# Kernel tuning notes

Measured on AMD Instinct MI355X. Metric: run time of the kernel, lower is better.

## Reference

```python
import jax, jax.numpy as jnp
import numpy as np

B, N, D_IN, D_OUT = 2, 2048, 2048, 2048
H, G = 16, 4            # num_heads, n_kv_groups
HD = D_OUT // H         # head_dim = 128
REP = H // G            # query heads per kv head = 4


def setup_inputs() -> dict:
    key = jax.random.key(0)
    ks = jax.random.split(key, 6)
    s = lambda fan_in: 1.0 / np.sqrt(fan_in)
    return {
        "x": jax.random.normal(ks[0], (B, N, D_IN), jnp.float32),
        "Wq": jax.random.normal(ks[1], (D_IN, D_OUT), jnp.float32) * s(D_IN),
        "Wk": jax.random.normal(ks[2], (D_IN, G * HD), jnp.float32) * s(D_IN),
        "Wv": jax.random.normal(ks[3], (D_IN, G * HD), jnp.float32) * s(D_IN),
        "Wo": jax.random.normal(ks[4], (D_OUT, D_OUT), jnp.float32) * s(D_OUT),
        "bo": jnp.zeros((D_OUT,), jnp.float32),
    }


def reference(x, Wq, Wk, Wv, Wo, bo):
    b, n, _ = x.shape
    # projections
    q = (x @ Wq).reshape(b, n, G, REP, HD)   # query heads grouped: h = g*REP + r
    k = (x @ Wk).reshape(b, n, G, HD)
    v = (x @ Wv).reshape(b, n, G, HD)
    # grouped attention scores; KV broadcast over REP instead of repeat_kv
    scores = jnp.einsum('bqgrd,bkgd->bgrqk', q, k)  # [b,G,REP,N,N]
    causal = jnp.tril(jnp.ones((n, n), bool))       # allowed positions
    scores = jnp.where(causal, scores, -jnp.inf)
    w = jax.nn.softmax(scores / np.float32(np.sqrt(HD)), axis=-1)
    ctx = jnp.einsum('bgrqk,bkgd->bqgrd', w, v).reshape(b, n, D_OUT)
    return ctx @ Wo + bo
```

## Files before the change

kernel.cpp:

```cpp
#include <hip/hip_runtime.h>
#include <stdint.h>

typedef __attribute__((ext_vector_type(8))) __bf16 bf16x8;
typedef __attribute__((ext_vector_type(4))) float f32x4;
typedef __attribute__((ext_vector_type(4))) short short4v;

static constexpr int SEQ  = 2048;
static constexpr int DQKV = 3072;
static constexpr int HD   = 128;

__device__ __forceinline__ short f2bf(float f) {
  unsigned u = __builtin_bit_cast(unsigned, f);
  u += 0x7fffu + ((u >> 16) & 1u);
  return (short)(u >> 16);
}

__device__ __forceinline__ unsigned pack2(float a, float b) {
  return (unsigned)(unsigned short)f2bf(a) | ((unsigned)(unsigned short)f2bf(b) << 16);
}

__device__ __forceinline__ void gl_lds16(const void* g, void* l) {
  __builtin_amdgcn_global_load_lds(
      (const __attribute__((address_space(1))) void*)g,
      (__attribute__((address_space(3))) void*)l, 16, 0, 0);
}

__global__ __launch_bounds__(256)
void prep_kernel(const float* __restrict__ x, const float* __restrict__ Wq,
                 const float* __restrict__ Wk, const float* __restrict__ Wv,
                 const float* __restrict__ Wo,
                 short* __restrict__ xb, short* __restrict__ WqkvT,
                 short* __restrict__ WoT) {
  int blk = blockIdx.x, tid = threadIdx.x;
  if (blk < 8192) {
    int i = blk * 256 + tid;
    float4 v = reinterpret_cast<const float4*>(x)[i];
    short4v o;
    o[0] = f2bf(v.x); o[1] = f2bf(v.y); o[2] = f2bf(v.z); o[3] = f2bf(v.w);
    *reinterpret_cast<short4v*>(xb + (size_t)i * 4) = o;
    return;
  }
  blk -= 8192;
  __shared__ float tile[32][33];
  const float* in; short* out; int C, bx, by;
  if (blk < 4096)      { in = Wq; out = WqkvT;                     C = 2048; bx = blk & 63; by = blk >> 6; }
  else if (blk < 5120) { int t = blk - 4096; in = Wk; out = WqkvT + (size_t)2048 * 2048; C = 512; bx = t & 15; by = t >> 4; }
  else if (blk < 6144) { int t = blk - 5120; in = Wv; out = WqkvT + (size_t)2560 * 2048; C = 512; bx = t & 15; by = t >> 4; }
  else                 { int t = blk - 6144; in = Wo; out = WoT;   C = 2048; bx = t & 63; by = t >> 6; }
  const int R = 2048;
  int c0 = bx * 32, r0 = by * 32, tx = tid & 31, ty = tid >> 5;
  for (int i = 0; i < 4; i++)
    tile[ty + i * 8][tx] = in[(size_t)(r0 + ty + i * 8) * C + c0 + tx];
  __syncthreads();
  for (int i = 0; i < 4; i++)
    out[(size_t)(c0 + ty + i * 8) * R + r0 + tx] = f2bf(tile[tx][ty + i * 8]);
}

__global__ __launch_bounds__(256) void transpose_v_kernel(const short* __restrict__ qkv,
                                                          short* __restrict__ vT) {
  __shared__ short tile[32][33];
  int n0 = blockIdx.x * 32, c0 = blockIdx.y * 32, b = blockIdx.z;
  int tx = threadIdx.x & 31, ty = threadIdx.x >> 5;
  for (int i = 0; i < 4; i++)
    tile[ty + i * 8][tx] = qkv[(size_t)(b * SEQ + n0 + ty + i * 8) * DQKV + 2560 + c0 + tx];
  __syncthreads();
  for (int i = 0; i < 4; i++)
    vT[(size_t)(b * 512 + c0 + ty + i * 8) * SEQ + n0 + tx] = tile[tx][ty + i * 8];
}

template <int F32OUT>
__global__ __launch_bounds__(256)
void gemm_bt_kernel(const short* __restrict__ A, const short* __restrict__ BT,
                    void* __restrict__ Cout, const float* __restrict__ bias,
                    int M, int N, int K, int qcols, float qscale) {
  __shared__ __align__(16) short As[8192];
  __shared__ __align__(16) short Bs[8192];
  const int tid = threadIdx.x, lane = tid & 63, w = tid >> 6;
  const int l15 = lane & 15, quad = lane >> 4, q8 = quad * 8;
  const int row0 = blockIdx.y * 128, col0 = blockIdx.x * 128;
  const int wm = (w >> 1) * 64, wn = (w & 1) * 64;
  f32x4 acc[4][4] = {};
  const short* ga0 = A  + (size_t)(row0 + w * 16 + (lane >> 2)) * K + (lane & 3) * 8;
  const short* gb0 = BT + (size_t)(col0 + w * 16 + (lane >> 2)) * K + (lane & 3) * 8;
  for (int kt = 0; kt < K; kt += 64) {
    for (int s = 0; s < 2; s++) {
      gl_lds16(ga0 + kt + s * 32,                  As + s * 4096 + w * 512);
      gl_lds16(ga0 + (size_t)64 * K + kt + s * 32, As + s * 4096 + 2048 + w * 512);
      gl_lds16(gb0 + kt + s * 32,                  Bs + s * 4096 + w * 512);
      gl_lds16(gb0 + (size_t)64 * K + kt + s * 32, Bs + s * 4096 + 2048 + w * 512);
    }
    __syncthreads();
    for (int s = 0; s < 2; s++) {
      bf16x8 af[4], bfr[4];
      for (int i = 0; i < 4; i++)
        af[i] = *reinterpret_cast<const bf16x8*>(As + s * 4096 + (wm + i * 16 + l15) * 32 + q8);
      for (int j = 0; j < 4; j++)
        bfr[j] = *reinterpret_cast<const bf16x8*>(Bs + s * 4096 + (wn + j * 16 + l15) * 32 + q8);
      for (int i = 0; i < 4; i++)
        for (int j = 0; j < 4; j++)
          acc[i][j] = __builtin_amdgcn_mfma_f32_16x16x32_bf16(af[i], bfr[j], acc[i][j], 0, 0, 0);
    }
    __syncthreads();
  }
  if (F32OUT) {
    float* C = (float*)Cout;
    for (int j = 0; j < 4; j++) {
      int col = col0 + wn + j * 16 + l15;
      float bv = bias[col];
      for (int i = 0; i < 4; i++)
        for (int r = 0; r < 4; r++)
          C[(size_t)(row0 + wm + i * 16 + quad * 4 + r) * N + col] = acc[i][j][r] + bv;
    }
  } else {
    short* C = (short*)Cout;
    for (int j = 0; j < 4; j++) {
      int col = col0 + wn + j * 16 + l15;
      float sc = (col < qcols) ? qscale : 1.0f;
      for (int i = 0; i < 4; i++)
        for (int r = 0; r < 4; r++)
          C[(size_t)(row0 + wm + i * 16 + quad * 4 + r) * N + col] = f2bf(acc[i][j][r] * sc);
    }
  }
}

__global__ __launch_bounds__(256, 2)
void attn_kernel(const short* __restrict__ qkv, const short* __restrict__ vT,
                 short* __restrict__ ctx) {
  __shared__ __align__(16) short Ks[16384];
  __shared__ __align__(16) short Vs[16384];
  __shared__ __align__(16) short Ps[4096];
  const int tid = threadIdx.x, lane = tid & 63, w = tid >> 6;
  const int l15 = lane & 15, quad = lane >> 4, q8 = quad * 8;
  const int idx = blockIdx.x;
  const int p = idx >> 5, h = (idx >> 1) & 15, b = idx & 1, g = h >> 2;
  const int qtA = 31 - p, qtB = p;

  bf16x8 qf[2][4];
  for (int seg = 0; seg < 2; seg++) {
    const int qt = seg ? qtB : qtA;
    const short* gq = qkv + (size_t)(b * SEQ + qt * 64 + w * 16 + l15) * DQKV + h * HD + q8;
    for (int ds = 0; ds < 4; ds++)
      qf[seg][ds] = *reinterpret_cast<const bf16x8*>(gq + ds * 32);
  }
  bf16x8 ones;
  for (int i = 0; i < 8; i++) ones[i] = __builtin_bit_cast(__bf16, (short)0x3F80);

  f32x4 acco[8] = {};
  f32x4 accl = {};

  auto stage = [&](int buf, int kt) {
    const short* gk = qkv + (size_t)(b * SEQ + kt * 64 + w * 16 + (lane >> 2)) * DQKV +
                      2048 + g * HD + (lane & 3) * 8;
    for (int ks = 0; ks < 4; ks++)
      gl_lds16(gk + ks * 32, Ks + buf * 8192 + ks * 2048 + w * 512);
    for (int c = 0; c < 2; c++)
      for (int ih = 0; ih < 2; ih++)
        gl_lds16(vT + (size_t)(b * 512 + g * HD + ih * 64 + w * 16 + (lane >> 2)) * SEQ +
                     kt * 64 + c * 32 + (lane & 3) * 8,
                 Vs + buf * 8192 + c * 4096 + ih * 2048 + w * 512);
  };

  const int lenA = qtA + 1;
  const int total = lenA + qtB + 1;
  stage(0, 0);
  for (int t = 0; t < total; t++) {
    const int seg = (t >= lenA);
    const int kt = seg ? (t - lenA) : t;
    const int qt = seg ? qtB : qtA;
    const int cur = t & 1;
    __syncthreads();
    if (t + 1 < total) {
      const int nkt = (t + 1 >= lenA) ? (t + 1 - lenA) : (t + 1);
      stage(cur ^ 1, nkt);
    }

    const short* Kb = Ks + cur * 8192;
    const short* Vb = Vs + cur * 8192;

    f32x4 accs[4] = {};
    for (int ds = 0; ds < 4; ds++)
      for (int j = 0; j < 4; j++) {
        bf16x8 kf = *reinterpret_cast<const bf16x8*>(Kb + ds * 2048 + (j * 16 + l15) * 32 + q8);
        accs[j] = __builtin_amdgcn_mfma_f32_16x16x32_bf16(kf, qf[seg][ds], accs[j], 0, 0, 0);
      }

    if (kt == qt) {
      const int q = w * 16 + l15;
      for (int j = 0; j < 4; j++)
        for (int r = 0; r < 4; r++)
          if (j * 16 + quad * 4 + r > q) accs[j][r] = -1e38f;
    }

    for (int j = 0; j < 4; j++) {
      float p0 = exp2f(accs[j][0]), p1 = exp2f(accs[j][1]);
      float p2 = exp2f(accs[j][2]), p3 = exp2f(accs[j][3]);
      unsigned u0 = __builtin_bit_cast(unsigned, p0), u1 = __builtin_bit_cast(unsigned, p1);
      unsigned u2 = __builtin_bit_cast(unsigned, p2), u3 = __builtin_bit_cast(unsigned, p3);
      uint2 dd = make_uint2((u0 >> 16) | (u1 & 0xffff0000u),
                            (u2 >> 16) | (u3 & 0xffff0000u));
      const int chw = (2 * j + (quad >> 1)) ^ (l15 & 7);
      *reinterpret_cast<uint2*>(Ps + w * 1024 + l15 * 64 + chw * 8 + (quad & 1) * 4) = dd;
    }
    asm volatile("s_waitcnt lgkmcnt(0)" ::: "memory");

    for (int c = 0; c < 2; c++) {
      const int chr = (4 * c + quad) ^ (l15 & 7);
      bf16x8 pf = *reinterpret_cast<const bf16x8*>(Ps + w * 1024 + l15 * 64 + chr * 8);
      accl = __builtin_amdgcn_mfma_f32_16x16x32_bf16(ones, pf, accl, 0, 0, 0);
      for (int nt = 0; nt < 8; nt++) {
        bf16x8 vf = *reinterpret_cast<const bf16x8*>(Vb + c * 4096 + (nt * 16 + l15) * 32 + q8);
        acco[nt] = __builtin_amdgcn_mfma_f32_16x16x32_bf16(vf, pf, acco[nt], 0, 0, 0);
      }
    }

    if (kt == qt) {
      const float invl = 1.f / accl[0];
      const size_t row = (size_t)(b * SEQ + qt * 64 + w * 16 + l15);
      for (int nt = 0; nt < 8; nt++) {
        uint2 dd = make_uint2(pack2(acco[nt][0] * invl, acco[nt][1] * invl),
                              pack2(acco[nt][2] * invl, acco[nt][3] * invl));
        *reinterpret_cast<uint2*>(ctx + row * 2048 + h * HD + nt * 16 + quad * 4) = dd;
      }
      for (int nt = 0; nt < 8; nt++) acco[nt] = f32x4{0.f, 0.f, 0.f, 0.f};
      accl = f32x4{0.f, 0.f, 0.f, 0.f};
    }
  }
}

extern "C" void kernel_launch(void* const* d_in, const int* in_sizes, int n_in,
                              void* d_out, int out_size, void* d_ws, size_t ws_size,
                              hipStream_t stream) {
  const float* x  = (const float*)d_in[0];
  const float* Wq = (const float*)d_in[1];
  const float* Wk = (const float*)d_in[2];
  const float* Wv = (const float*)d_in[3];
  const float* Wo = (const float*)d_in[4];
  const float* bo = (const float*)d_in[5];
  float* out = (float*)d_out;

  const float sc2 = 0.08838834764831845f * 1.4426950408889634f;

  short* xb    = (short*)d_ws;
  short* WqkvT = xb    + (size_t)4096 * 2048;
  short* WoT   = WqkvT + (size_t)3072 * 2048;
  short* qkv   = WoT   + (size_t)2048 * 2048;
  short* vT    = qkv   + (size_t)4096 * 3072;
  short* ctx   = vT    + (size_t)1024 * 2048;

  prep_kernel<<<dim3(18432), dim3(256), 0, stream>>>(x, Wq, Wk, Wv, Wo, xb, WqkvT, WoT);
  gemm_bt_kernel<0><<<dim3(24, 32), dim3(256), 0, stream>>>(xb, WqkvT, qkv, nullptr,
                                                            4096, 3072, 2048, 2048, sc2);
  transpose_v_kernel<<<dim3(64, 16, 2), dim3(256), 0, stream>>>(qkv, vT);
  attn_kernel<<<dim3(512), dim3(256), 0, stream>>>(qkv, vT, ctx);
  gemm_bt_kernel<1><<<dim3(16, 32), dim3(256), 0, stream>>>(ctx, WoT, out, bo,
                                                            4096, 2048, 2048, 0, 1.0f);
}
```

Before: 299.4 us.

## Restructure attention to 32x32 MFMA with split-K waves and register P

Rewrites the attention kernel to use 32x32x16 MFMA tiles. Each wave now handles a 32-query by 32-key quadrant, and two key-half waves are reduced through LDS at the end of each query tile. V is loaded straight from global into registers instead of being staged in LDS. P is converted to a B operand with permlane32_swap rather than a round trip through LDS, and the row sum is accumulated with scalar adds instead of a ones-MFMA. The aim is to cut LDS traffic and instruction count, at the cost of uncached global V loads on the critical path, an extra barrier and reduction per query tile, and more register pressure.

```diff
diff --git a/kernel.cpp b/kernel.cpp
--- a/kernel.cpp
+++ b/kernel.cpp
@@ -3,7 +3,9 @@
 
 typedef __attribute__((ext_vector_type(8))) __bf16 bf16x8;
 typedef __attribute__((ext_vector_type(4))) float f32x4;
+typedef __attribute__((ext_vector_type(16))) float f32x16;
 typedef __attribute__((ext_vector_type(4))) short short4v;
+typedef __attribute__((ext_vector_type(4))) unsigned uint4v;
 
 static constexpr int SEQ  = 2048;
 static constexpr int DQKV = 3072;
@@ -126,43 +128,32 @@
 __global__ __launch_bounds__(256, 2)
 void attn_kernel(const short* __restrict__ qkv, const short* __restrict__ vT,
                  short* __restrict__ ctx) {
-  __shared__ __align__(16) short Ks[16384];
-  __shared__ __align__(16) short Vs[16384];
-  __shared__ __align__(16) short Ps[4096];
+  __shared__ __align__(16) short Ks[2 * 8192];
+  __shared__ __align__(16) float Oex[2 * 4096];
+  __shared__ float lbuf[4 * 32];
   const int tid = threadIdx.x, lane = tid & 63, w = tid >> 6;
-  const int l15 = lane & 15, quad = lane >> 4, q8 = quad * 8;
+  const int l31 = lane & 31, hi = lane >> 5;
+  const int qh = w & 1, kh = w >> 1;
   const int idx = blockIdx.x;
   const int p = idx >> 5, h = (idx >> 1) & 15, b = idx & 1, g = h >> 2;
   const int qtA = 31 - p, qtB = p;
-
-  bf16x8 qf[2][4];
-  for (int seg = 0; seg < 2; seg++) {
-    const int qt = seg ? qtB : qtA;
-    const short* gq = qkv + (size_t)(b * SEQ + qt * 64 + w * 16 + l15) * DQKV + h * HD + q8;
-    for (int ds = 0; ds < 4; ds++)
-      qf[seg][ds] = *reinterpret_cast<const bf16x8*>(gq + ds * 32);
-  }
-  bf16x8 ones;
-  for (int i = 0; i < 8; i++) ones[i] = __builtin_bit_cast(__bf16, (short)0x3F80);
-
-  f32x4 acco[8] = {};
-  f32x4 accl = {};
-
-  auto stage = [&](int buf, int kt) {
-    const short* gk = qkv + (size_t)(b * SEQ + kt * 64 + w * 16 + (lane >> 2)) * DQKV +
-                      2048 + g * HD + (lane & 3) * 8;
-    for (int ks = 0; ks < 4; ks++)
-      gl_lds16(gk + ks * 32, Ks + buf * 8192 + ks * 2048 + w * 512);
-    for (int c = 0; c < 2; c++)
-      for (int ih = 0; ih < 2; ih++)
-        gl_lds16(vT + (size_t)(b * 512 + g * HD + ih * 64 + w * 16 + (lane >> 2)) * SEQ +
-                     kt * 64 + c * 32 + (lane & 3) * 8,
-                 Vs + buf * 8192 + c * 4096 + ih * 2048 + w * 512);
+  const int lenA = qtA + 1, total = lenA + qtB + 1;
+
+  auto stageK = [&](int buf, int kt) {
+    const short* gk = qkv + (size_t)(b * SEQ + kt * 64) * DQKV + 2048 + g * HD;
+#pragma unroll
+    for (int s = 0; s < 4; s++) {
+      const int r = w * 16 + s * 4 + (lane >> 4);
+      gl_lds16(gk + (size_t)r * DQKV + ((lane & 15) ^ (r & 7)) * 8,
+               Ks + buf * 8192 + (w * 16 + s * 4) * 128);
+    }
   };
 
-  const int lenA = qtA + 1;
-  const int total = lenA + qtB + 1;
-  stage(0, 0);
+  bf16x8 qf[8];
+  f32x16 o_acc[4] = {};
+  float lsum = 0.f;
+
+  stageK(0, 0);
   for (int t = 0; t < total; t++) {
     const int seg = (t >= lenA);
     const int kt = seg ? (t - lenA) : t;
@@ -171,58 +162,110 @@
     __syncthreads();
     if (t + 1 < total) {
       const int nkt = (t + 1 >= lenA) ? (t + 1 - lenA) : (t + 1);
-      stage(cur ^ 1, nkt);
-    }
+      stageK(cur ^ 1, nkt);
+    }
+    if (t == 0 || t == lenA) {
+      const short* gq = qkv + (size_t)(b * SEQ + qt * 64 + qh * 32 + l31) * DQKV + h * HD + hi * 8;
+#pragma unroll
+      for (int d = 0; d < 8; d++) qf[d] = *reinterpret_cast<const bf16x8*>(gq + d * 16);
+    }
+
+    bf16x8 vf[4][2];
+#pragma unroll
+    for (int dt = 0; dt < 4; dt++)
+#pragma unroll
+      for (int sub = 0; sub < 2; sub++)
+        vf[dt][sub] = *reinterpret_cast<const bf16x8*>(
+            vT + (size_t)(b * 512 + g * HD + dt * 32 + l31) * SEQ +
+            kt * 64 + (kh * 2 + sub) * 16 + hi * 8);
 
     const short* Kb = Ks + cur * 8192;
-    const short* Vb = Vs + cur * 8192;
-
-    f32x4 accs[4] = {};
-    for (int ds = 0; ds < 4; ds++)
-      for (int j = 0; j < 4; j++) {
-        bf16x8 kf = *reinterpret_cast<const bf16x8*>(Kb + ds * 2048 + (j * 16 + l15) * 32 + q8);
-        accs[j] = __builtin_amdgcn_mfma_f32_16x16x32_bf16(kf, qf[seg][ds], accs[j], 0, 0, 0);
+    f32x16 sa = {};
+#pragma unroll
+    for (int d = 0; d < 8; d++) {
+      bf16x8 kf = *reinterpret_cast<const bf16x8*>(
+          Kb + (kh * 32 + l31) * 128 + (((d * 2 + hi) ^ (l31 & 7)) * 8));
+      sa = __builtin_amdgcn_mfma_f32_32x32x16_bf16(kf, qf[d], sa, 0, 0, 0);
+    }
+
+    if (kt == qt) {
+      const int q = qh * 32 + l31;
+#pragma unroll
+      for (int r = 0; r < 16; r++)
+        if (kh * 32 + (r & 3) + 8 * (r >> 2) + 4 * hi > q) sa[r] = -1e38f;
+    }
+
+    float ps[16];
+#pragma unroll
+    for (int r = 0; r < 16; r++) ps[r] = exp2f(sa[r]);
+#pragma unroll
+    for (int r = 0; r < 16; r++) lsum += ps[r];
+    unsigned ub[4][2];
+#pragma unroll
+    for (int j = 0; j < 4; j++) {
+      unsigned a0 = __builtin_bit_cast(unsigned, ps[4 * j + 0]);
+      unsigned a1 = __builtin_bit_cast(unsigned, ps[4 * j + 1]);
+      unsigned a2 = __builtin_bit_cast(unsigned, ps[4 * j + 2]);
+      unsigned a3 = __builtin_bit_cast(unsigned, ps[4 * j + 3]);
+      ub[j][0] = (a0 >> 16) | (a1 & 0xffff0000u);
+      ub[j][1] = (a2 >> 16) | (a3 & 0xffff0000u);
+    }
+    bf16x8 pfrag[2];
+#pragma unroll
+    for (int sub = 0; sub < 2; sub++) {
+      auto s0 = __builtin_amdgcn_permlane32_swap((int)ub[2 * sub][0], (int)ub[2 * sub + 1][0], false, false);
+      auto s1 = __builtin_amdgcn_permlane32_swap((int)ub[2 * sub][1], (int)ub[2 * sub + 1][1], false, false);
+      uint4v uu;
+      uu[0] = (unsigned)s0[0]; uu[1] = (unsigned)s1[0];
+      uu[2] = (unsigned)s0[1]; uu[3] = (unsigned)s1[1];
+      pfrag[sub] = __builtin_bit_cast(bf16x8, uu);
+    }
+
+    __builtin_amdgcn_s_setprio(1);
+#pragma unroll
+    for (int dt = 0; dt < 4; dt++)
+#pragma unroll
+      for (int sub = 0; sub < 2; sub++)
+        o_acc[dt] = __builtin_amdgcn_mfma_f32_32x32x16_bf16(vf[dt][sub], pfrag[sub], o_acc[dt], 0, 0, 0);
+    __builtin_amdgcn_s_setprio(0);
+
+    if (kt == qt) {
+      float lp = lsum + __shfl_xor(lsum, 32, 64);
+      if (lane < 32) lbuf[w * 32 + l31] = lp;
+      if (w >= 2) {
+        float* oex = Oex + (w - 2) * 4096;
+#pragma unroll
+        for (int dt = 0; dt < 4; dt++)
+#pragma unroll
+          for (int rq = 0; rq < 4; rq++) {
+            f32x4 vv = {o_acc[dt][4 * rq + 0], o_acc[dt][4 * rq + 1],
+                        o_acc[dt][4 * rq + 2], o_acc[dt][4 * rq + 3]};
+            *reinterpret_cast<f32x4*>(oex + ((dt * 4 + rq) * 64 + lane) * 4) = vv;
+          }
       }
-
-    if (kt == qt) {
-      const int q = w * 16 + l15;
-      for (int j = 0; j < 4; j++)
-        for (int r = 0; r < 4; r++)
-          if (j * 16 + quad * 4 + r > q) accs[j][r] = -1e38f;
-    }
-
-    for (int j = 0; j < 4; j++) {
-      float p0 = exp2f(accs[j][0]), p1 = exp2f(accs[j][1]);
-      float p2 = exp2f(accs[j][2]), p3 = exp2f(accs[j][3]);
-      unsigned u0 = __builtin_bit_cast(unsigned, p0), u1 = __builtin_bit_cast(unsigned, p1);
-      unsigned u2 = __builtin_bit_cast(unsigned, p2), u3 = __builtin_bit_cast(unsigned, p3);
-      uint2 dd = make_uint2((u0 >> 16) | (u1 & 0xffff0000u),
-                            (u2 >> 16) | (u3 & 0xffff0000u));
-      const int chw = (2 * j + (quad >> 1)) ^ (l15 & 7);
-      *reinterpret_cast<uint2*>(Ps + w * 1024 + l15 * 64 + chw * 8 + (quad & 1) * 4) = dd;
-    }
-    asm volatile("s_waitcnt lgkmcnt(0)" ::: "memory");
-
-    for (int c = 0; c < 2; c++) {
-      const int chr = (4 * c + quad) ^ (l15 & 7);
-      bf16x8 pf = *reinterpret_cast<const bf16x8*>(Ps + w * 1024 + l15 * 64 + chr * 8);
-      accl = __builtin_amdgcn_mfma_f32_16x16x32_bf16(ones, pf, accl, 0, 0, 0);
-      for (int nt = 0; nt < 8; nt++) {
-        bf16x8 vf = *reinterpret_cast<const bf16x8*>(Vb + c * 4096 + (nt * 16 + l15) * 32 + q8);
-        acco[nt] = __builtin_amdgcn_mfma_f32_16x16x32_bf16(vf, pf, acco[nt], 0, 0, 0);
+      __syncthreads();
+      if (w < 2) {
+        const float invl = 1.f / (lp + lbuf[(w ^ 2) * 32 + l31]);
+        const float* oex = Oex + w * 4096;
+        const size_t row = (size_t)(b * SEQ + qt * 64 + qh * 32 + l31);
+#pragma unroll
+        for (int dt = 0; dt < 4; dt++)
+#pragma unroll
+          for (int rq = 0; rq < 4; rq++) {
+            f32x4 vv = *reinterpret_cast<const f32x4*>(oex + ((dt * 4 + rq) * 64 + lane) * 4);
+            float e0 = (o_acc[dt][4 * rq + 0] + vv[0]) * invl;
+            float e1 = (o_acc[dt][4 * rq + 1] + vv[1]) * invl;
+            float e2 = (o_acc[dt][4 * rq + 2] + vv[2]) * invl;
+            float e3 = (o_acc[dt][4 * rq + 3] + vv[3]) * invl;
+            uint2 dd = make_uint2(pack2(e0, e1), pack2(e2, e3));
+            *reinterpret_cast<uint2*>(ctx + row * 2048 + h * HD + dt * 32 + rq * 8 + hi * 4) = dd;
+          }
       }
-    }
-
-    if (kt == qt) {
-      const float invl = 1.f / accl[0];
-      const size_t row = (size_t)(b * SEQ + qt * 64 + w * 16 + l15);
-      for (int nt = 0; nt < 8; nt++) {
-        uint2 dd = make_uint2(pack2(acco[nt][0] * invl, acco[nt][1] * invl),
-                              pack2(acco[nt][2] * invl, acco[nt][3] * invl));
-        *reinterpret_cast<uint2*>(ctx + row * 2048 + h * HD + nt * 16 + quad * 4) = dd;
-      }
-      for (int nt = 0; nt < 8; nt++) acco[nt] = f32x4{0.f, 0.f, 0.f, 0.f};
-      accl = f32x4{0.f, 0.f, 0.f, 0.f};
+#pragma unroll
+      for (int dt = 0; dt < 4; dt++)
+#pragma unroll
+        for (int e = 0; e < 16; e++) o_acc[dt][e] = 0.f;
+      lsum = 0.f;
     }
   }
 }
```

New measurement: 310.3 us. +3.6%, slower.

## Rework attention kernel with 32x32 MFMA, split-K waves and software-pipelined QK/PV

Applied to the files above, without the earlier changes.

Rewrites the attention inner loop to use 32x32x16 MFMA tiles. The four waves are split into 2 query halves by 2 key halves. The P matrix is transposed in registers with permlane32_swap instead of a round-trip through LDS, and the row sum is kept as a scalar accumulator rather than computed with a ones-MFMA. QK^T for the next tile is software-pipelined against softmax/PV of the previous tile, with swizzled LDS layouts and setprio hints. The key-split partial outputs are reduced through shared memory at diagonal tiles. This adds extra barriers and LDS traffic at each diagonal, plus higher register pressure.

```diff
diff --git a/kernel.cpp b/kernel.cpp
--- a/kernel.cpp
+++ b/kernel.cpp
@@ -3,7 +3,9 @@
 
 typedef __attribute__((ext_vector_type(8))) __bf16 bf16x8;
 typedef __attribute__((ext_vector_type(4))) float f32x4;
+typedef __attribute__((ext_vector_type(16))) float f32x16;
 typedef __attribute__((ext_vector_type(4))) short short4v;
+typedef __attribute__((ext_vector_type(4))) unsigned uint4v;
 
 static constexpr int SEQ  = 2048;
 static constexpr int DQKV = 3072;
@@ -126,105 +128,187 @@
 __global__ __launch_bounds__(256, 2)
 void attn_kernel(const short* __restrict__ qkv, const short* __restrict__ vT,
                  short* __restrict__ ctx) {
-  __shared__ __align__(16) short Ks[16384];
-  __shared__ __align__(16) short Vs[16384];
-  __shared__ __align__(16) short Ps[4096];
+  __shared__ __align__(16) short Ks[2 * 8192];
+  __shared__ __align__(16) short Vs[2 * 8192];
+  __shared__ __align__(16) float Oex[2048];
+  __shared__ float lbuf[4 * 32];
   const int tid = threadIdx.x, lane = tid & 63, w = tid >> 6;
-  const int l15 = lane & 15, quad = lane >> 4, q8 = quad * 8;
+  const int l31 = lane & 31, hi = lane >> 5;
+  const int qh = w & 1, kh = w >> 1;
   const int idx = blockIdx.x;
   const int p = idx >> 5, h = (idx >> 1) & 15, b = idx & 1, g = h >> 2;
   const int qtA = 31 - p, qtB = p;
-
-  bf16x8 qf[2][4];
-  for (int seg = 0; seg < 2; seg++) {
-    const int qt = seg ? qtB : qtA;
-    const short* gq = qkv + (size_t)(b * SEQ + qt * 64 + w * 16 + l15) * DQKV + h * HD + q8;
-    for (int ds = 0; ds < 4; ds++)
-      qf[seg][ds] = *reinterpret_cast<const bf16x8*>(gq + ds * 32);
-  }
-  bf16x8 ones;
-  for (int i = 0; i < 8; i++) ones[i] = __builtin_bit_cast(__bf16, (short)0x3F80);
-
-  f32x4 acco[8] = {};
-  f32x4 accl = {};
+  const int lenA = qtA + 1;
 
   auto stage = [&](int buf, int kt) {
-    const short* gk = qkv + (size_t)(b * SEQ + kt * 64 + w * 16 + (lane >> 2)) * DQKV +
-                      2048 + g * HD + (lane & 3) * 8;
-    for (int ks = 0; ks < 4; ks++)
-      gl_lds16(gk + ks * 32, Ks + buf * 8192 + ks * 2048 + w * 512);
-    for (int c = 0; c < 2; c++)
-      for (int ih = 0; ih < 2; ih++)
-        gl_lds16(vT + (size_t)(b * 512 + g * HD + ih * 64 + w * 16 + (lane >> 2)) * SEQ +
-                     kt * 64 + c * 32 + (lane & 3) * 8,
-                 Vs + buf * 8192 + c * 4096 + ih * 2048 + w * 512);
+    const short* gk = qkv + (size_t)(b * SEQ + kt * 64) * DQKV + 2048 + g * HD;
+#pragma unroll
+    for (int s = 0; s < 4; s++) {
+      const int r = w * 16 + s * 4 + (lane >> 4);
+      gl_lds16(gk + (size_t)r * DQKV + ((lane & 15) ^ (r & 7)) * 8,
+               Ks + buf * 8192 + (w * 16 + s * 4) * 128);
+    }
+    const short* gv = vT + (size_t)(b * 512 + g * HD) * SEQ + kt * 64;
+#pragma unroll
+    for (int s = 0; s < 4; s++) {
+      const int r = w * 32 + s * 8 + (lane >> 3);
+      gl_lds16(gv + (size_t)r * SEQ + ((lane & 7) ^ (r & 7)) * 8,
+               Vs + buf * 8192 + (w * 32 + s * 8) * 64);
+    }
   };
 
-  const int lenA = qtA + 1;
-  const int total = lenA + qtB + 1;
+  bf16x8 qf[8];
+  f32x16 o_acc[4] = {};
+  float lsum = 0.f;
+  f32x16 saA, saB;
+  bf16x8 vfA[4][2], vfB[4][2];
+
+  auto loadQ = [&](int qt) {
+    const short* gq = qkv + (size_t)(b * SEQ + qt * 64 + qh * 32 + l31) * DQKV + h * HD + hi * 8;
+#pragma unroll
+    for (int d = 0; d < 8; d++) qf[d] = *reinterpret_cast<const bf16x8*>(gq + d * 16);
+  };
+
+#define PH1_BODY(T, CUR, SA, VF)                                                   \
+  {                                                                                \
+    if ((T) == 0 || (T) == lenA) loadQ(((T) >= lenA) ? qtB : qtA);                 \
+    const short* Kb_ = Ks + (CUR) * 8192;                                          \
+    const short* Vb_ = Vs + (CUR) * 8192;                                          \
+    f32x16 s0_ = {}, s1_ = {};                                                     \
+    __builtin_amdgcn_s_setprio(1);                                                 \
+    _Pragma("unroll")                                                              \
+    for (int d_ = 0; d_ < 4; d_++) {                                               \
+      bf16x8 kf0_ = *reinterpret_cast<const bf16x8*>(                              \
+          Kb_ + (kh * 32 + l31) * 128 + (((2 * d_ + hi) ^ (l31 & 7)) * 8));        \
+      bf16x8 kf1_ = *reinterpret_cast<const bf16x8*>(                              \
+          Kb_ + (kh * 32 + l31) * 128 + (((2 * (d_ + 4) + hi) ^ (l31 & 7)) * 8));  \
+      s0_ = __builtin_amdgcn_mfma_f32_32x32x16_bf16(kf0_, qf[d_], s0_, 0, 0, 0);   \
+      s1_ = __builtin_amdgcn_mfma_f32_32x32x16_bf16(kf1_, qf[d_ + 4], s1_, 0, 0, 0);\
+    }                                                                              \
+    __builtin_amdgcn_s_setprio(0);                                                 \
+    SA = s0_ + s1_;                                                                \
+    _Pragma("unroll")                                                              \
+    for (int dt_ = 0; dt_ < 4; dt_++)                                              \
+      _Pragma("unroll")                                                            \
+      for (int sub_ = 0; sub_ < 2; sub_++) {                                       \
+        const int kc_ = kh * 4 + sub_ * 2 + hi;                                    \
+        VF[dt_][sub_] = *reinterpret_cast<const bf16x8*>(                          \
+            Vb_ + (dt_ * 32 + l31) * 64 + ((kc_ ^ (l31 & 7)) * 8));                \
+      }                                                                            \
+  }
+
+#define PH2_BODY(T, SA, VF)                                                        \
+  {                                                                                \
+    const int seg_ = ((T) >= lenA);                                                \
+    const int ktc_ = seg_ ? (T) - lenA : (T);                                      \
+    const int qtc_ = seg_ ? qtB : qtA;                                             \
+    const bool diag_ = (ktc_ == qtc_);                                             \
+    if (diag_) {                                                                   \
+      const int q_ = qh * 32 + l31;                                                \
+      _Pragma("unroll")                                                            \
+      for (int r_ = 0; r_ < 16; r_++)                                              \
+        if (kh * 32 + (r_ & 3) + 8 * (r_ >> 2) + 4 * hi > q_) SA[r_] = -1e38f;     \
+    }                                                                              \
+    float ps_[16];                                                                 \
+    _Pragma("unroll")                                                              \
+    for (int r_ = 0; r_ < 16; r_++)                                                \
+      asm("v_exp_f32 %0, %1" : "=v"(ps_[r_]) : "v"(SA[r_]));                       \
+    _Pragma("unroll")                                                              \
+    for (int r_ = 0; r_ < 16; r_++) lsum += ps_[r_];                               \
+    unsigned ub_[4][2];                                                            \
+    _Pragma("unroll")                                                              \
+    for (int j_ = 0; j_ < 4; j_++) {                                               \
+      unsigned a0_ = __builtin_bit_cast(unsigned, ps_[4 * j_ + 0]);                \
+      unsigned a1_ = __builtin_bit_cast(unsigned, ps_[4 * j_ + 1]);                \
+      unsigned a2_ = __builtin_bit_cast(unsigned, ps_[4 * j_ + 2]);                \
+      unsigned a3_ = __builtin_bit_cast(unsigned, ps_[4 * j_ + 3]);                \
+      ub_[j_][0] = (a0_ >> 16) | (a1_ & 0xffff0000u);                              \
+      ub_[j_][1] = (a2_ >> 16) | (a3_ & 0xffff0000u);                              \
+    }                                                                              \
+    bf16x8 pf_[2];                                                                 \
+    _Pragma("unroll")                                                              \
+    for (int sub_ = 0; sub_ < 2; sub_++) {                                         \
+      auto s0_ = __builtin_amdgcn_permlane32_swap((int)ub_[2 * sub_][0],           \
+                                                  (int)ub_[2 * sub_ + 1][0], false, false); \
+      auto s1_ = __builtin_amdgcn_permlane32_swap((int)ub_[2 * sub_][1],           \
+                                                  (int)ub_[2 * sub_ + 1][1], false, false); \
+      uint4v uu_;                                                                  \
+      uu_[0] = (unsigned)s0_[0]; uu_[1] = (unsigned)s1_[0];                        \
+      uu_[2] = (unsigned)s0_[1]; uu_[3] = (unsigned)s1_[1];                        \
+      pf_[sub_] = __builtin_bit_cast(bf16x8, uu_);                                 \
+    }                                                                              \
+    __builtin_amdgcn_s_setprio(1);                                                 \
+    _Pragma("unroll")                                                              \
+    for (int dt_ = 0; dt_ < 4; dt_++)                                              \
+      _Pragma("unroll")                                                            \
+      for (int sub_ = 0; sub_ < 2; sub_++)                                         \
+        o_acc[dt_] = __builtin_amdgcn_mfma_f32_32x32x16_bf16(VF[dt_][sub_], pf_[sub_], \
+                                                             o_acc[dt_], 0, 0, 0); \
+    __builtin_amdgcn_s_setprio(0);                                                 \
+    if (diag_) {                                                                   \
+      float lp_ = lsum + __shfl_xor(lsum, 32, 64);                                 \
+      if (lane < 32) lbuf[w * 32 + l31] = lp_;                                     \
+      float invl_ = 0.f;                                                           \
+      const size_t row_ = (size_t)(b * SEQ + qtc_ * 64 + qh * 32 + l31);           \
+      _Pragma("unroll")                                                            \
+      for (int dt_ = 0; dt_ < 4; dt_++) {                                          \
+        if (w >= 2) {                                                              \
+          float* oex_ = Oex + (w - 2) * 1024;                                      \
+          _Pragma("unroll")                                                        \
+          for (int rq_ = 0; rq_ < 4; rq_++) {                                      \
+            f32x4 vv_ = {o_acc[dt_][4 * rq_ + 0], o_acc[dt_][4 * rq_ + 1],         \
+                         o_acc[dt_][4 * rq_ + 2], o_acc[dt_][4 * rq_ + 3]};        \
+            *reinterpret_cast<f32x4*>(oex_ + (rq_ * 64 + lane) * 4) = vv_;         \
+          }                                                                        \
+        }                                                                          \
+        __syncthreads();                                                           \
+        if (w < 2) {                                                               \
+          if (dt_ == 0) invl_ = 1.f / (lp_ + lbuf[(w ^ 2) * 32 + l31]);            \
+          const float* oex_ = Oex + w * 1024;                                      \
+          _Pragma("unroll")                                                        \
+          for (int rq_ = 0; rq_ < 4; rq_++) {                                      \
+            f32x4 vv_ = *reinterpret_cast<const f32x4*>(oex_ + (rq_ * 64 + lane) * 4); \
+            float e0_ = (o_acc[dt_][4 * rq_ + 0] + vv_[0]) * invl_;                \
+            float e1_ = (o_acc[dt_][4 * rq_ + 1] + vv_[1]) * invl_;                \
+            float e2_ = (o_acc[dt_][4 * rq_ + 2] + vv_[2]) * invl_;                \
+            float e3_ = (o_acc[dt_][4 * rq_ + 3] + vv_[3]) * invl_;                \
+            uint2 dd_ = make_uint2(pack2(e0_, e1_), pack2(e2_, e3_));              \
+            *reinterpret_cast<uint2*>(ctx + row_ * 2048 + h * HD + dt_ * 32 +      \
+                                      rq_ * 8 + hi * 4) = dd_;                     \
+          }                                                                        \
+        }                                                                          \
+        __syncthreads();                                                           \
+      }                                                                            \
+      _Pragma("unroll")                                                            \
+      for (int dt_ = 0; dt_ < 4; dt_++)                                            \
+        _Pragma("unroll")                                                          \
+        for (int e_ = 0; e_ < 16; e_++) o_acc[dt_][e_] = 0.f;                      \
+      lsum = 0.f;                                                                  \
+    }                                                                              \
+  }
+
   stage(0, 0);
-  for (int t = 0; t < total; t++) {
-    const int seg = (t >= lenA);
-    const int kt = seg ? (t - lenA) : t;
-    const int qt = seg ? qtB : qtA;
-    const int cur = t & 1;
+  __syncthreads();
+  stage(1, (1 >= lenA) ? 1 - lenA : 1);
+  __builtin_amdgcn_sched_barrier(0);
+  PH1_BODY(0, 0, saA, vfA)
+
+  for (int tb = 1; tb <= 31; tb += 2) {
     __syncthreads();
-    if (t + 1 < total) {
-      const int nkt = (t + 1 >= lenA) ? (t + 1 - lenA) : (t + 1);
-      stage(cur ^ 1, nkt);
-    }
-
-    const short* Kb = Ks + cur * 8192;
-    const short* Vb = Vs + cur * 8192;
-
-    f32x4 accs[4] = {};
-    for (int ds = 0; ds < 4; ds++)
-      for (int j = 0; j < 4; j++) {
-        bf16x8 kf = *reinterpret_cast<const bf16x8*>(Kb + ds * 2048 + (j * 16 + l15) * 32 + q8);
-        accs[j] = __builtin_amdgcn_mfma_f32_16x16x32_bf16(kf, qf[seg][ds], accs[j], 0, 0, 0);
-      }
-
-    if (kt == qt) {
-      const int q = w * 16 + l15;
-      for (int j = 0; j < 4; j++)
-        for (int r = 0; r < 4; r++)
-          if (j * 16 + quad * 4 + r > q) accs[j][r] = -1e38f;
-    }
-
-    for (int j = 0; j < 4; j++) {
-      float p0 = exp2f(accs[j][0]), p1 = exp2f(accs[j][1]);
-      float p2 = exp2f(accs[j][2]), p3 = exp2f(accs[j][3]);
-      unsigned u0 = __builtin_bit_cast(unsigned, p0), u1 = __builtin_bit_cast(unsigned, p1);
-      unsigned u2 = __builtin_bit_cast(unsigned, p2), u3 = __builtin_bit_cast(unsigned, p3);
-      uint2 dd = make_uint2((u0 >> 16) | (u1 & 0xffff0000u),
-                            (u2 >> 16) | (u3 & 0xffff0000u));
-      const int chw = (2 * j + (quad >> 1)) ^ (l15 & 7);
-      *reinterpret_cast<uint2*>(Ps + w * 1024 + l15 * 64 + chw * 8 + (quad & 1) * 4) = dd;
-    }
-    asm volatile("s_waitcnt lgkmcnt(0)" ::: "memory");
-
-    for (int c = 0; c < 2; c++) {
-      const int chr = (4 * c + quad) ^ (l15 & 7);
-      bf16x8 pf = *reinterpret_cast<const bf16x8*>(Ps + w * 1024 + l15 * 64 + chr * 8);
-      accl = __builtin_amdgcn_mfma_f32_16x16x32_bf16(ones, pf, accl, 0, 0, 0);
-      for (int nt = 0; nt < 8; nt++) {
-        bf16x8 vf = *reinterpret_cast<const bf16x8*>(Vb + c * 4096 + (nt * 16 + l15) * 32 + q8);
-        acco[nt] = __builtin_amdgcn_mfma_f32_16x16x32_bf16(vf, pf, acco[nt], 0, 0, 0);
-      }
-    }
-
-    if (kt == qt) {
-      const float invl = 1.f / accl[0];
-      const size_t row = (size_t)(b * SEQ + qt * 64 + w * 16 + l15);
-      for (int nt = 0; nt < 8; nt++) {
-        uint2 dd = make_uint2(pack2(acco[nt][0] * invl, acco[nt][1] * invl),
-                              pack2(acco[nt][2] * invl, acco[nt][3] * invl));
-        *reinterpret_cast<uint2*>(ctx + row * 2048 + h * HD + nt * 16 + quad * 4) = dd;
-      }
-      for (int nt = 0; nt < 8; nt++) acco[nt] = f32x4{0.f, 0.f, 0.f, 0.f};
-      accl = f32x4{0.f, 0.f, 0.f, 0.f};
-    }
-  }
+    { const int tn = tb + 1; stage(0, (tn >= lenA) ? tn - lenA : tn); }
+    __builtin_amdgcn_sched_barrier(0);
+    PH1_BODY(tb, 1, saB, vfB)
+    PH2_BODY(tb - 1, saA, vfA)
+    __syncthreads();
+    if (tb + 2 < 33) { const int tn = tb + 2; stage(1, (tn >= lenA) ? tn - lenA : tn); }
+    __builtin_amdgcn_sched_barrier(0);
+    PH1_BODY(tb + 1, 0, saA, vfA)
+    PH2_BODY(tb, saB, vfB)
+  }
+  PH2_BODY(32, saA, vfA)
+
+#undef PH1_BODY
+#undef PH2_BODY
 }
 
 extern "C" void kernel_launch(void* const* d_in, const int* in_sizes, int n_in,
```

After: 359.8 us. 1.2x slower.
